# Kernel tuning notes

Measured on AMD Instinct MI355X. Metric: run time of the kernel, lower is better.

Reference implementation:

```python
import jax, jax.numpy as jnp
import numpy as np

N = 10000        # nodes
F_IN = 128       # node features (data.num_node_features)
OUT = 16         # out_channels
H = 32           # attention heads
C1 = 4 * OUT     # hidden per-head dim (4*out_channels)
E = 80000        # directed edges
EPS = 1e-5       # BatchNorm eps
NEG = 0.2        # GATConv LeakyReLU negative_slope


def _gat(x, src, dst, W, a_s, a_d, b, n, C):
    # PyG GATConv, shared lin, concat=False (mean over heads)
    h = (x @ W).reshape(n, H, C)                    # [n,H,C]
    e_src = jnp.sum(h * a_s, -1)                    # [n,H] (alpha from x_j)
    e_dst = jnp.sum(h * a_d, -1)                    # [n,H] (alpha from x_i)
    e = jax.nn.leaky_relu(e_src[src] + e_dst[dst], NEG)     # [E',H]
    m = jax.ops.segment_max(e, dst, num_segments=n)         # segment softmax
    p = jnp.exp(e - m[dst])
    z = jax.ops.segment_sum(p, dst, num_segments=n)
    alpha = p / z[dst]
    out = jax.ops.segment_sum(alpha[:, :, None] * h[src], dst, num_segments=n)
    return out.mean(1) + b                          # mean over heads + bias


def _bn(x, g, b, m, v):  # eval-mode BatchNorm1d (running stats)
    return (x - m) * g / jnp.sqrt(v + EPS) + b


def setup_inputs():
    k = jax.random.split(jax.random.key(0), 40)
    rn = lambda i, s, sc=0.1: jax.random.normal(k[i], s, jnp.float32) * sc
    d = {"x": jax.random.normal(k[0], (N, F_IN), jnp.float32),
         "edge_index": jax.random.randint(k[1], (2, E), 0, N, jnp.int32)}
    # 4 GATConv layers
    d.update(W1=rn(2, (F_IN, H * C1)), as1=rn(3, (H, C1)), ad1=rn(4, (H, C1)), b1=rn(5, (C1,)))
    d.update(W2=rn(6, (C1, H * OUT)), as2=rn(7, (H, OUT)), ad2=rn(8, (H, OUT)), b2=rn(9, (OUT,)))
    d.update(W3=rn(10, (F_IN, H * C1)), as3=rn(11, (H, C1)), ad3=rn(12, (H, C1)), b3=rn(13, (C1,)))
    d.update(W4=rn(14, (C1, H * OUT)), as4=rn(15, (H, OUT)), ad4=rn(16, (H, OUT)), b4=rn(17, (OUT,)))
    # ResidualNetwork(1 block): 1x1 Conv1d over L=1 == matmul
    d.update(rwa=rn(18, (F_IN, OUT)), rba=rn(19, (OUT,)),
             bn1g=jnp.ones(OUT), bn1b=jnp.zeros(OUT), bn1m=rn(20, (OUT,)), bn1v=jnp.abs(rn(21, (OUT,))) + 1.0,
             rwb=rn(22, (OUT, OUT)), rbb=rn(23, (OUT,)),
             bn2g=jnp.ones(OUT), bn2b=jnp.zeros(OUT), bn2m=rn(24, (OUT,)), bn2v=jnp.abs(rn(25, (OUT,))) + 1.0,
             wsc=rn(26, (F_IN, OUT)), bsc=rn(27, (OUT,)),
             bnsg=jnp.ones(OUT), bnsb=jnp.zeros(OUT), bnsm=rn(28, (OUT,)), bnsv=jnp.abs(rn(29, (OUT,))) + 1.0,
             wfc=rn(30, (OUT, OUT)), bfc=rn(31, (OUT,)))
    return d


def reference(x, edge_index, W1, as1, ad1, b1, W2, as2, ad2, b2,
              W3, as3, ad3, b3, W4, as4, ad4, b4,
              rwa, rba, bn1g, bn1b, bn1m, bn1v, rwb, rbb, bn2g, bn2b, bn2m, bn2v,
              wsc, bsc, bnsg, bnsb, bnsm, bnsv, wfc, bfc):
    n = x.shape[0]
    loops = jnp.arange(n, dtype=edge_index.dtype)  # add_self_loops=True
    s2t_src = jnp.concatenate([edge_index[0], loops])  # flow source_to_target
    s2t_dst = jnp.concatenate([edge_index[1], loops])
    t2s_src = jnp.concatenate([edge_index[1], loops])  # flow target_to_source
    t2s_dst = jnp.concatenate([edge_index[0], loops])
    # dropout in original is unassigned (no-op); eval mode assumed
    x_s = jax.nn.elu(_gat(x, s2t_src, s2t_dst, W1, as1, ad1, b1, n, C1))
    x_in = jax.nn.elu(_gat(x_s, s2t_src, s2t_dst, W2, as2, ad2, b2, n, OUT))
    x_t = jax.nn.elu(_gat(x, t2s_src, t2s_dst, W3, as3, ad3, b3, n, C1))
    x_out = jax.nn.elu(_gat(x_t, t2s_src, t2s_dst, W4, as4, ad4, b4, n, OUT))
    # ResidualNetwork: block + identity avg-pool (L=1) + fc
    h = jax.nn.relu(_bn(x @ rwa + rba, bn1g, bn1b, bn1m, bn1v))
    h = _bn(h @ rwb + rbb, bn2g, bn2b, bn2m, bn2v)
    sc = _bn(x @ wsc + bsc, bnsg, bnsb, bnsm, bnsv)
    x_self = jax.nn.relu(h + sc) @ wfc + bfc
    return (x_in, x_out, x_self)
```

## Files before the change

### kernel.cpp

```cpp
#include <hip/hip_runtime.h>
#include <stdint.h>

__device__ __forceinline__ float bf2f(unsigned short u) {
  union { unsigned int i; float f; } v; v.i = ((unsigned int)u) << 16; return v.f;
}
__device__ __forceinline__ unsigned short f2bf(float f) {
  union { float f; unsigned int i; } v; v.f = f;
  unsigned int i = v.i;
  unsigned int r = (i + 0x7fffu + ((i >> 16) & 1u)) >> 16;
  return (unsigned short)r;
}

typedef __bf16 bf16x8 __attribute__((ext_vector_type(8)));
typedef float f32x4 __attribute__((ext_vector_type(4)));
typedef float f32x2 __attribute__((ext_vector_type(2)));
union ABfrag { int4 i4; bf16x8 v; };

#if __has_builtin(__builtin_amdgcn_cvt_pk_fp8_f32) && __has_builtin(__builtin_amdgcn_cvt_pk_f32_fp8)
#define HW_FP8 1
#else
#define HW_FP8 0
#endif

__device__ __forceinline__ unsigned char f2fp8_sw(float f) {
  union { float f; unsigned int u; } v; v.f = f;
  unsigned int s = (v.u >> 24) & 0x80;
  float a = fabsf(f);
  if (a >= 448.f) return (unsigned char)(s | 0x7E);
  v.f = a;
  int ex = (int)(v.u >> 23);
  unsigned int man = v.u & 0x7FFFFFu;
  if (ex >= 121) {
    unsigned int val = ((unsigned int)(ex - 120) << 3) | (man >> 20);
    unsigned int rem = man & 0xFFFFFu;
    if (rem > 0x80000u || (rem == 0x80000u && (val & 1))) val++;
    if (val > 0x7E) val = 0x7E;
    return (unsigned char)(s | val);
  }
  int q = (int)(a * 512.f + 0.5f);
  if (q > 8) q = 8;
  return (unsigned char)(s | (unsigned int)q);
}
__device__ __forceinline__ float fp8dec_sw(unsigned char c) {
  unsigned int e = (c >> 3) & 15u, m = c & 7u;
  float v;
  if (e) { union { unsigned int u; float f; } x; x.u = ((e + 120) << 23) | (m << 20); v = x.f; }
  else v = (float)m * 0.001953125f;
  return (c & 0x80) ? -v : v;
}
__device__ __forceinline__ unsigned char f2fp8(float f) {
#if HW_FP8
  int v = __builtin_amdgcn_cvt_pk_fp8_f32(f, f, 0, false);
  return (unsigned char)(v & 0xFF);
#else
  return f2fp8_sw(f);
#endif
}
__device__ __forceinline__ void dec16p(int4 g, f32x2 o[8]) {
#if HW_FP8
  o[0] = __builtin_amdgcn_cvt_pk_f32_fp8(g.x, false);
  o[1] = __builtin_amdgcn_cvt_pk_f32_fp8(g.x, true);
  o[2] = __builtin_amdgcn_cvt_pk_f32_fp8(g.y, false);
  o[3] = __builtin_amdgcn_cvt_pk_f32_fp8(g.y, true);
  o[4] = __builtin_amdgcn_cvt_pk_f32_fp8(g.z, false);
  o[5] = __builtin_amdgcn_cvt_pk_f32_fp8(g.z, true);
  o[6] = __builtin_amdgcn_cvt_pk_f32_fp8(g.w, false);
  o[7] = __builtin_amdgcn_cvt_pk_f32_fp8(g.w, true);
#else
  unsigned int w[4] = {(unsigned)g.x, (unsigned)g.y, (unsigned)g.z, (unsigned)g.w};
#pragma unroll
  for (int d = 0; d < 4; ++d) {
    unsigned int x = w[d];
    o[d * 2 + 0] = (f32x2){fp8dec_sw((unsigned char)(x & 0xFF)),
                           fp8dec_sw((unsigned char)((x >> 8) & 0xFF))};
    o[d * 2 + 1] = (f32x2){fp8dec_sw((unsigned char)((x >> 16) & 0xFF)),
                           fp8dec_sw((unsigned char)((x >> 24) & 0xFF))};
  }
#endif
}

__device__ __forceinline__ float lrelu_clamp(float e) {
  e = (e > 0.f) ? e : 0.2f * e;
  return fminf(e, 80.f);
}

__global__ __launch_bounds__(256) void k_detect(const unsigned int* __restrict__ x, int* flag,
                                                int* __restrict__ degAB, int ndeg2) {
  if (blockIdx.x == 0) {
    __shared__ int cnt;
    if (threadIdx.x == 0) cnt = 0;
    __syncthreads();
    int c = 0;
    for (int i = threadIdx.x; i < 1024; i += 256) {
      unsigned int lo = x[i] & 0xFFFFu;
      int ex = (int)((lo >> 7) & 0xFF);
      if (ex >= 100 && ex <= 140) c++;
    }
    atomicAdd(&cnt, c);
    __syncthreads();
    if (threadIdx.x == 0) flag[0] = (cnt > 600) ? 1 : 0;
    return;
  }
  for (int idx = (blockIdx.x - 1) * 256 + threadIdx.x; idx < ndeg2; idx += 8 * 256) degAB[idx] = 0;
}

struct PrepDesc {
  const void* csrc[32]; float* cdst[32]; int cn[32];
  const void* x; float* xc; unsigned short* xp;
  const void* W1; const void* W2; const void* W3; const void* W4;
  unsigned short* P1; unsigned short* P2; unsigned short* P3; unsigned short* P4;
  int* degAB;
  const int* ei;
  int nxb, xtotal, ctotal, E, nn;
};
__global__ __launch_bounds__(256) void k_prep(PrepDesc d, const int* __restrict__ flag) {
  int isbf = *flag;
  int b = blockIdx.x;
  if (b < d.nxb) {
    int i = b * 256 + threadIdx.x;
    if (i < d.xtotal) {
      float v = isbf ? bf2f(((const unsigned short*)d.x)[i]) : ((const float*)d.x)[i];
      d.xc[i] = v;
      int row = i >> 7, c = i & 127;
      int tm = row >> 4, mr = row & 15;
      int s = c >> 5, quad = (c >> 3) & 3, j = c & 7;
      size_t idx = (((size_t)tm * 4 + s) * 64 + quad * 16 + mr) * 8 + j;
      d.xp[idx] = f2bf(v);
    }
    return;
  }
  b -= d.nxb;
  if (b < 288) {
    int u = b * 256 + threadIdx.x;
    const void* W; unsigned short* P; int K, N, lu;
    if (u < 32768)      { W = d.W1; P = d.P1; K = 128; N = 2048; lu = u; }
    else if (u < 36864) { W = d.W2; P = d.P2; K = 64;  N = 512;  lu = u - 32768; }
    else if (u < 69632) { W = d.W3; P = d.P3; K = 128; N = 2048; lu = u - 36864; }
    else                { W = d.W4; P = d.P4; K = 64;  N = 512;  lu = u - 69632; }
    int ksteps = K >> 5;
    int g = lu / (ksteps * 64);
    int rem = lu - g * (ksteps * 64);
    int s = rem >> 6, lane = rem & 63;
    int mr = lane & 15, quad = lane >> 4;
    int col = g * 16 + mr;
    int kbase = s * 32 + quad * 8;
#pragma unroll
    for (int j = 0; j < 8; ++j) {
      size_t src = (size_t)(kbase + j) * N + col;
      float v = isbf ? bf2f(((const unsigned short*)W)[src]) : ((const float*)W)[src];
      P[(size_t)lu * 8 + j] = f2bf(v);
    }
    return;
  }
  b -= 288;
  if (b < 4) {
    for (int idx = b * 256 + threadIdx.x; idx < d.ctotal; idx += 4 * 256) {
      int t = 0, off = idx;
      while (off >= d.cn[t]) { off -= d.cn[t]; ++t; }
      float v = isbf ? bf2f(((const unsigned short*)d.csrc[t])[off])
                     : ((const float*)d.csrc[t])[off];
      d.cdst[t][off] = v;
    }
    return;
  }
  b -= 4;
  {
    int e = b * 256 + threadIdx.x;
    if (e < d.E) {
      atomicAdd(&d.degAB[d.ei[d.E + e]], 1);
      atomicAdd(&d.degAB[d.nn + d.ei[e]], 1);
    }
  }
}

__global__ __launch_bounds__(1024) void k_exscan2(const int* __restrict__ degA, const int* __restrict__ degB,
                                                  int* __restrict__ rowA, int* __restrict__ rowB,
                                                  int* __restrict__ colA, int* __restrict__ colB,
                                                  int* __restrict__ curA, int* __restrict__ curB, int n) {
  const int* deg = (blockIdx.x == 0) ? degA : degB;
  int* row = (blockIdx.x == 0) ? rowA : rowB;
  int* colx = (blockIdx.x == 0) ? colA : colB;
  int* curx = (blockIdx.x == 0) ? curA : curB;
  __shared__ int wsum[16], wbase[16];
  __shared__ int carry;
  if (threadIdx.x == 0) carry = 0;
  __syncthreads();
  int lane = threadIdx.x & 63, w = threadIdx.x >> 6;
  int chunks = (n + 1023) >> 10;
  for (int ch = 0; ch < chunks; ++ch) {
    int i = (ch << 10) + threadIdx.x;
    int v = (i < n) ? deg[i] : 0;
    int sc = v;
#pragma unroll
    for (int o = 1; o < 64; o <<= 1) { int t = __shfl_up(sc, o); if (lane >= o) sc += t; }
    if (lane == 63) wsum[w] = sc;
    __syncthreads();
    if (threadIdx.x < 16) {
      int v2 = wsum[threadIdx.x], s2 = v2;
#pragma unroll
      for (int o = 1; o < 16; o <<= 1) { int t = __shfl_up(s2, o); if (lane >= o) s2 += t; }
      wbase[threadIdx.x] = s2 - v2;
      if (threadIdx.x == 15) wsum[15] = s2;
    }
    __syncthreads();
    if (i < n) {
      int rv = carry + wbase[w] + (sc - v) + i;
      row[i] = rv;
      colx[rv] = i;
      curx[i] = rv + 1;
    }
    __syncthreads();
    if (threadIdx.x == 0) carry += wsum[15];
    __syncthreads();
  }
  if (threadIdx.x == 0) row[n] = carry + n;
}

union SMem {
  struct { int4 a[1024]; unsigned char tile[4][16][64]; } mm;
  struct { float xs[16][128]; float ha[16][16]; float tt[16][16]; } res;
};

template<int CH, int KSTEPS>
__device__ __forceinline__ void mm_es64_body(int rg, int cg, int MT,
    const unsigned short* __restrict__ Ap, const unsigned short* __restrict__ Bp,
    unsigned char* __restrict__ C, const float* __restrict__ a_s, const float* __restrict__ a_d,
    float* __restrict__ es, float* __restrict__ ed, int N, SMem* sm) {
  const int TI = KSTEPS * 64;
  int vt = MT - rg * 4; if (vt > 4) vt = 4;
  {
    const int4* src = (const int4*)(Ap + (size_t)rg * 4 * TI * 8);
    int tot = vt * TI;
    for (int t = threadIdx.x; t < tot; t += 256) sm->mm.a[t] = src[t];
  }
  __syncthreads();
  int wid = threadIdx.x >> 6;
  int tn = cg * 4 + wid;
  int lane = threadIdx.x & 63;
  int mr = lane & 15, quad = lane >> 4;
  const unsigned short* bp = Bp + ((size_t)tn * 4 * KSTEPS) * 512 + lane * 8;
  f32x4 acc[4][4];
#pragma unroll
  for (int rt = 0; rt < 4; ++rt)
#pragma unroll
    for (int nt = 0; nt < 4; ++nt) acc[rt][nt] = (f32x4){0.f, 0.f, 0.f, 0.f};
#pragma unroll
  for (int s = 0; s < KSTEPS; ++s) {
    ABfrag bfr[4];
#pragma unroll
    for (int nt = 0; nt < 4; ++nt) bfr[nt].i4 = *(const int4*)(bp + (size_t)(nt * KSTEPS + s) * 512);
    ABfrag afr[4];
#pragma unroll
    for (int rt = 0; rt < 4; ++rt) afr[rt].i4 = sm->mm.a[rt * TI + s * 64 + lane];
#pragma unroll
    for (int nt = 0; nt < 4; ++nt)
#pragma unroll
      for (int rt = 0; rt < 4; ++rt)
        acc[rt][nt] = __builtin_amdgcn_mfma_f32_16x16x32_bf16(afr[rt].v, bfr[nt].v, acc[rt][nt], 0, 0, 0);
  }
  int r16 = lane >> 2, seg = lane & 3;
#pragma unroll
  for (int rt = 0; rt < 4; ++rt) {
    if (rt < vt) {
      int tm = rg * 4 + rt;
#pragma unroll
      for (int nt = 0; nt < 4; ++nt)
#pragma unroll
        for (int r = 0; r < 4; ++r)
          sm->mm.tile[wid][quad * 4 + r][nt * 16 + mr] = f2fp8(acc[rt][nt][r]);
      int4 val = *(const int4*)&sm->mm.tile[wid][r16][seg * 16];
      *(int4*)(C + (size_t)(tm * 16 + r16) * N + tn * 64 + seg * 16) = val;
    }
  }
  if (CH == 64) {
    const float* asr = a_s + tn * 64;
    const float* adr = a_d + tn * 64;
    float ws[4], wd[4];
#pragma unroll
    for (int nt = 0; nt < 4; ++nt) { ws[nt] = asr[nt * 16 + mr]; wd[nt] = adr[nt * 16 + mr]; }
#pragma unroll
    for (int rt = 0; rt < 4; ++rt) {
      if (rt < vt) {
        int tm = rg * 4 + rt;
        float pes[4] = {0.f,0.f,0.f,0.f}, ped[4] = {0.f,0.f,0.f,0.f};
#pragma unroll
        for (int nt = 0; nt < 4; ++nt)
#pragma unroll
          for (int r = 0; r < 4; ++r) { pes[r] += acc[rt][nt][r] * ws[nt]; ped[r] += acc[rt][nt][r] * wd[nt]; }
#pragma unroll
        for (int m = 1; m < 16; m <<= 1)
#pragma unroll
          for (int r = 0; r < 4; ++r) {
            pes[r] += __shfl_xor(pes[r], m);
            ped[r] += __shfl_xor(ped[r], m);
          }
        if (mr == 0) {
#pragma unroll
          for (int r = 0; r < 4; ++r) {
            int row = tm * 16 + quad * 4 + r;
            es[row * 32 + tn] = pes[r];
            ed[row * 32 + tn] = ped[r];
          }
        }
      }
    }
  } else {
    float ws[4], wd[4];
#pragma unroll
    for (int nt = 0; nt < 4; ++nt) {
      ws[nt] = a_s[(tn * 4 + nt) * 16 + mr];
      wd[nt] = a_d[(tn * 4 + nt) * 16 + mr];
    }
#pragma unroll
    for (int rt = 0; rt < 4; ++rt) {
      if (rt < vt) {
        int tm = rg * 4 + rt;
        float pes[4][4], ped[4][4];
#pragma unroll
        for (int nt = 0; nt < 4; ++nt)
#pragma unroll
          for (int r = 0; r < 4; ++r) { pes[nt][r] = acc[rt][nt][r] * ws[nt]; ped[nt][r] = acc[rt][nt][r] * wd[nt]; }
#pragma unroll
        for (int m = 1; m < 16; m <<= 1)
#pragma unroll
          for (int nt = 0; nt < 4; ++nt)
#pragma unroll
            for (int r = 0; r < 4; ++r) {
              pes[nt][r] += __shfl_xor(pes[nt][r], m);
              ped[nt][r] += __shfl_xor(ped[nt][r], m);
            }
        if (mr == 0) {
#pragma unroll
          for (int nt = 0; nt < 4; ++nt)
#pragma unroll
            for (int r = 0; r < 4; ++r) {
              int row = tm * 16 + quad * 4 + r;
              es[row * 32 + tn * 4 + nt] = pes[nt][r];
              ed[row * 32 + tn * 4 + nt] = ped[nt][r];
            }
        }
      }
    }
  }
}

struct MM13Desc {
  const unsigned short* Ap;
  const unsigned short* B1; const unsigned short* B3;
  unsigned char* C1; unsigned char* C3;
  const float* as1; const float* ad1; const float* as3; const float* ad3;
  float* es1; float* ed1; float* es3; float* ed3;
  int sblks, mmblks, E, mt;
  const int* ei; int* colA; int* colB; int* curA; int* curB;
  const float* xc;
  const float* rp[20];
  void* outbase; size_t eoff; int n;
  const int* flag;
};
__global__ __launch_bounds__(256) void k_mm13res(MM13Desc d) {
  __shared__ SMem sm;
  int b = blockIdx.x;
  if (b < d.sblks) {
    int e = b * 256 + threadIdx.x;
    if (e < d.E) {
      int s = d.ei[e], dd = d.ei[d.E + e];
      d.colA[atomicAdd(&d.curA[dd], 1)] = s;
      d.colB[atomicAdd(&d.curB[s], 1)] = dd;
    }
    return;
  }
  b -= d.sblks;
  if (b < d.mmblks) {
    mm_es64_body<64,4>(b >> 3, b & 7, d.mt, d.Ap, d.B1, d.C1, d.as1, d.ad1, d.es1, d.ed1, 2048, &sm);
    return;
  }
  b -= d.mmblks;
  if (b < d.mmblks) {
    mm_es64_body<64,4>(b >> 3, b & 7, d.mt, d.Ap, d.B3, d.C3, d.as3, d.ad3, d.es3, d.ed3, 2048, &sm);
    return;
  }
  b -= d.mmblks;
  int nodebase = b * 16;
  for (int t = threadIdx.x; t < 16 * 128; t += 256)
    sm.res.xs[t >> 7][t & 127] = d.xc[(size_t)(nodebase + (t >> 7)) * 128 + (t & 127)];
  __syncthreads();
  int ni = threadIdx.x >> 4, c = threadIdx.x & 15;
  const float* rwa = d.rp[0]; const float* rba = d.rp[1];
  const float* bn1g = d.rp[2]; const float* bn1b = d.rp[3];
  const float* bn1m = d.rp[4]; const float* bn1v = d.rp[5];
  const float* rwb = d.rp[6]; const float* rbb = d.rp[7];
  const float* bn2g = d.rp[8]; const float* bn2b = d.rp[9];
  const float* bn2m = d.rp[10]; const float* bn2v = d.rp[11];
  const float* wsc = d.rp[12]; const float* bsc = d.rp[13];
  const float* bnsg = d.rp[14]; const float* bnsb = d.rp[15];
  const float* bnsm = d.rp[16]; const float* bnsv = d.rp[17];
  const float* wfc = d.rp[18]; const float* bfc = d.rp[19];
  float ya = 0.f, ysc = 0.f;
  for (int k = 0; k < 128; ++k) {
    float xv = sm.res.xs[ni][k];
    ya  += xv * rwa[k * 16 + c];
    ysc += xv * wsc[k * 16 + c];
  }
  ya += rba[c]; ysc += bsc[c];
  float s1 = bn1g[c] * rsqrtf(bn1v[c] + 1e-5f);
  ya = (ya - bn1m[c]) * s1 + bn1b[c];
  ya = fmaxf(ya, 0.f);
  float ss = bnsg[c] * rsqrtf(bnsv[c] + 1e-5f);
  ysc = (ysc - bnsm[c]) * ss + bnsb[c];
  sm.res.ha[ni][c] = ya;
  __syncthreads();
  float h2 = rbb[c];
  for (int k = 0; k < 16; ++k) h2 += sm.res.ha[ni][k] * rwb[k * 16 + c];
  float s2 = bn2g[c] * rsqrtf(bn2v[c] + 1e-5f);
  h2 = (h2 - bn2m[c]) * s2 + bn2b[c];
  sm.res.tt[ni][c] = fmaxf(h2 + ysc, 0.f);
  __syncthreads();
  float o = bfc[c];
  for (int k = 0; k < 16; ++k) o += sm.res.tt[ni][k] * wfc[k * 16 + c];
  size_t oo = d.eoff + (size_t)(nodebase + ni) * 16 + c;
  if (*d.flag) ((unsigned short*)d.outbase)[oo] = f2bf(o);
  else         ((float*)d.outbase)[oo] = o;
}

__global__ __launch_bounds__(256) void k_g64(const unsigned char* __restrict__ h1,
                                             const unsigned char* __restrict__ h3,
                                             const float* __restrict__ es1, const float* __restrict__ ed1,
                                             const float* __restrict__ es3, const float* __restrict__ ed3,
                                             const int* __restrict__ rowA, const int* __restrict__ colA,
                                             const int* __restrict__ rowB, const int* __restrict__ colB,
                                             const float* __restrict__ b1, const float* __restrict__ b3,
                                             unsigned short* __restrict__ xsp, unsigned short* __restrict__ xtp,
                                             int n, int gb) {
  int b = blockIdx.x;
  const unsigned char* h; const float *es, *ed, *bias; const int *rowp, *col; unsigned short* outp;
  if (b < gb) { h = h1; es = es1; ed = ed1; rowp = rowA; col = colA; bias = b1; outp = xsp; }
  else { b -= gb; h = h3; es = es3; ed = ed3; rowp = rowB; col = colB; bias = b3; outp = xtp; }
  int wid = threadIdx.x >> 6, lane = threadIdx.x & 63;
  int i = b * 4 + wid;
  if (i >= n) return;
  int hd0 = lane >> 2, hd1 = 16 + hd0;
  float e0 = ed[i * 32 + hd0];
  float e1 = ed[i * 32 + hd1];
  int beg = rowp[i], end = rowp[i + 1];
  int deg = end - beg;
  int colv = (lane < deg) ? col[beg + lane] : 0;
  f32x2 acc0[8], acc1[8];
#pragma unroll
  for (int k = 0; k < 8; ++k) { acc0[k] = (f32x2){0.f, 0.f}; acc1[k] = (f32x2){0.f, 0.f}; }
  float Z0 = 0.f, Z1 = 0.f;
  int s0 = __shfl(colv, 0);
  const int4* hp0 = (const int4*)(h + (size_t)s0 * 2048);
  int4 ng0 = hp0[lane];
  int4 ng1 = hp0[64 + lane];
  float na = es[s0 * 32 + hd0];
  float nb = es[s0 * 32 + hd1];
  for (int j = 0; j < deg; ++j) {
    int4 g0 = ng0, g1 = ng1;
    float ea = na, eb = nb;
    int jn = j + 1;
    if (jn < deg) {
      int sn = (jn < 64) ? __shfl(colv, jn) : col[beg + jn];
      const int4* hq = (const int4*)(h + (size_t)sn * 2048);
      ng0 = hq[lane];
      ng1 = hq[64 + lane];
      na = es[sn * 32 + hd0];
      nb = es[sn * 32 + hd1];
    }
    float q0 = __expf(lrelu_clamp(ea + e0));
    float q1 = __expf(lrelu_clamp(eb + e1));
    Z0 += q0; Z1 += q1;
    f32x2 d0[8], d1[8];
    dec16p(g0, d0); dec16p(g1, d1);
    f32x2 q0v = (f32x2){q0, q0}, q1v = (f32x2){q1, q1};
#pragma unroll
    for (int k = 0; k < 8; ++k) {
      acc0[k] = __builtin_elementwise_fma(q0v, d0[k], acc0[k]);
      acc1[k] = __builtin_elementwise_fma(q1v, d1[k], acc1[k]);
    }
  }
  float zi0 = 1.0f / Z0, zi1 = 1.0f / Z1;
  f32x2 zi0v = (f32x2){zi0, zi0}, zi1v = (f32x2){zi1, zi1};
  f32x2 v2[8];
#pragma unroll
  for (int k = 0; k < 8; ++k)
    v2[k] = __builtin_elementwise_fma(acc1[k], zi1v, acc0[k] * zi0v);
#pragma unroll
  for (int m = 4; m < 64; m <<= 1)
#pragma unroll
    for (int k = 0; k < 8; ++k) {
      v2[k].x += __shfl_xor(v2[k].x, m);
      v2[k].y += __shfl_xor(v2[k].y, m);
    }
  if (lane < 4) {
    float v[16];
#pragma unroll
    for (int k = 0; k < 8; ++k) { v[2 * k] = v2[k].x; v[2 * k + 1] = v2[k].y; }
    int tm = i >> 4, mr = i & 15;
    unsigned short ob[16];
#pragma unroll
    for (int k = 0; k < 16; ++k) {
      float t = v[k] * (1.f / 32.f) + bias[lane * 16 + k];
      t = (t > 0.f) ? t : (__expf(t) - 1.f);
      ob[k] = f2bf(t);
    }
    int s0w = lane >> 1;
#pragma unroll
    for (int g2 = 0; g2 < 2; ++g2) {
      size_t idx = (((size_t)tm * 2 + s0w) * 64 + ((lane & 1) * 2 + g2) * 16 + mr) * 8;
      *(int4*)(outp + idx) = *(const int4*)(ob + g2 * 8);
    }
  }
}

__global__ __launch_bounds__(256) void k_mm24(const unsigned short* __restrict__ xsp,
                                              const unsigned short* __restrict__ xtp,
                                              const unsigned short* __restrict__ W2p,
                                              const unsigned short* __restrict__ W4p,
                                              unsigned char* __restrict__ h2, unsigned char* __restrict__ h4,
                                              const float* __restrict__ as2, const float* __restrict__ ad2,
                                              const float* __restrict__ as4, const float* __restrict__ ad4,
                                              float* __restrict__ es2, float* __restrict__ ed2,
                                              float* __restrict__ es4, float* __restrict__ ed4,
                                              int mmblks, int mt) {
  __shared__ SMem sm;
  int b = blockIdx.x;
  if (b < mmblks)
    mm_es64_body<16,2>(b >> 1, b & 1, mt, xsp, W2p, h2, as2, ad2, es2, ed2, 512, &sm);
  else {
    b -= mmblks;
    mm_es64_body<16,2>(b >> 1, b & 1, mt, xtp, W4p, h4, as4, ad4, es4, ed4, 512, &sm);
  }
}

__global__ __launch_bounds__(256) void k_g16(const unsigned char* __restrict__ h2,
                                             const unsigned char* __restrict__ h4,
                                             const float* __restrict__ es2, const float* __restrict__ ed2,
                                             const float* __restrict__ es4, const float* __restrict__ ed4,
                                             const int* __restrict__ rowA, const int* __restrict__ colA,
                                             const int* __restrict__ rowB, const int* __restrict__ colB,
                                             const float* __restrict__ b2, const float* __restrict__ b4,
                                             void* __restrict__ outbase, int n, int gb,
                                             const int* __restrict__ flag) {
  int b = blockIdx.x;
  const unsigned char* h; const float *es, *ed, *bias; const int *rowp, *col; size_t eoff;
  if (b < gb) { h = h2; es = es2; ed = ed2; rowp = rowA; col = colA; bias = b2; eoff = 0; }
  else { b -= gb; h = h4; es = es4; ed = ed4; rowp = rowB; col = colB; bias = b4; eoff = (size_t)n * 16; }
  int wid = threadIdx.x >> 6, lane = threadIdx.x & 63;
  int i = b * 4 + wid;
  if (i >= n) return;
  int hh = lane & 31, j2 = lane >> 5;
  float ev = ed[i * 32 + hh];
  int beg = rowp[i], end = rowp[i + 1];
  int deg = end - beg;
  int colv = (lane < deg) ? col[beg + lane] : 0;
  f32x2 acc[8];
#pragma unroll
  for (int k = 0; k < 8; ++k) acc[k] = (f32x2){0.f, 0.f};
  float Z = 0.f;
  int j = j2;
  int4 ng = (int4){0, 0, 0, 0};
  float ne = 0.f;
  if (j < deg) {
    int s = __shfl(colv, j);
    ng = ((const int4*)(h + (size_t)s * 512))[hh];
    ne = es[s * 32 + hh];
  }
  for (; j < deg; j += 2) {
    int4 g = ng; float ee = ne;
    int jn = j + 2;
    if (jn < deg) {
      int sn = (jn < 64) ? __shfl(colv, jn) : col[beg + jn];
      ng = ((const int4*)(h + (size_t)sn * 512))[hh];
      ne = es[sn * 32 + hh];
    }
    float q = __expf(lrelu_clamp(ee + ev));
    Z += q;
    f32x2 d[8];
    dec16p(g, d);
    f32x2 qv = (f32x2){q, q};
#pragma unroll
    for (int k = 0; k < 8; ++k) acc[k] = __builtin_elementwise_fma(qv, d[k], acc[k]);
  }
  Z += __shfl_xor(Z, 32);
  float zi = 1.0f / Z;
  f32x2 ziv = (f32x2){zi, zi};
  f32x2 v2[8];
#pragma unroll
  for (int k = 0; k < 8; ++k) v2[k] = acc[k] * ziv;
#pragma unroll
  for (int m = 1; m < 64; m <<= 1)
#pragma unroll
    for (int k = 0; k < 8; ++k) {
      v2[k].x += __shfl_xor(v2[k].x, m);
      v2[k].y += __shfl_xor(v2[k].y, m);
    }
  if (lane == 0) {
    float v[16];
#pragma unroll
    for (int k = 0; k < 8; ++k) { v[2 * k] = v2[k].x; v[2 * k + 1] = v2[k].y; }
    int isbf = *flag;
    if (isbf) {
      unsigned short ob[16];
#pragma unroll
      for (int k = 0; k < 16; ++k) {
        float t = v[k] * (1.f / 32.f) + bias[k];
        t = (t > 0.f) ? t : (__expf(t) - 1.f);
        ob[k] = f2bf(t);
      }
      unsigned short* o = (unsigned short*)outbase + eoff + (size_t)i * 16;
      *(int4*)o = *(const int4*)ob;
      *(int4*)(o + 8) = *(const int4*)(ob + 8);
    } else {
      float* o = (float*)outbase + eoff + (size_t)i * 16;
#pragma unroll
      for (int k = 0; k < 16; ++k) {
        float t = v[k] * (1.f / 32.f) + bias[k];
        t = (t > 0.f) ? t : (__expf(t) - 1.f);
        o[k] = t;
      }
    }
  }
}

extern "C" void kernel_launch(void* const* d_in, const int* in_sizes, int n_in,
                              void* d_out, int out_size, void* d_ws, size_t ws_size,
                              hipStream_t stream) {
  const int n = in_sizes[0] / 128;
  const int E = in_sizes[1] / 2;
  const int* ei = (const int*)d_in[1];

  char* wsp = (char*)d_ws; size_t off = 0;
  auto alloc = [&](size_t bytes) -> void* {
    void* p = wsp + off; off = (off + bytes + 255) & ~(size_t)255; return p;
  };
  int* flag = (int*)alloc(4);
  float* xc = (float*)alloc((size_t)n * 128 * 4);
  unsigned short* xp = (unsigned short*)alloc((size_t)n * 128 * 2);
  unsigned short* W1p = (unsigned short*)alloc((size_t)2048 * 128 * 2);
  unsigned short* W2p = (unsigned short*)alloc((size_t)512 * 64 * 2);
  unsigned short* W3p = (unsigned short*)alloc((size_t)2048 * 128 * 2);
  unsigned short* W4p = (unsigned short*)alloc((size_t)512 * 64 * 2);
  unsigned char* h1 = (unsigned char*)alloc((size_t)n * 2048);
  unsigned char* h3 = (unsigned char*)alloc((size_t)n * 2048);
  unsigned char* h2 = (unsigned char*)alloc((size_t)n * 512);
  unsigned char* h4 = (unsigned char*)alloc((size_t)n * 512);
  float* es1 = (float*)alloc((size_t)n * 32 * 4);
  float* ed1 = (float*)alloc((size_t)n * 32 * 4);
  float* es3 = (float*)alloc((size_t)n * 32 * 4);
  float* ed3 = (float*)alloc((size_t)n * 32 * 4);
  float* es2 = (float*)alloc((size_t)n * 32 * 4);
  float* ed2 = (float*)alloc((size_t)n * 32 * 4);
  float* es4 = (float*)alloc((size_t)n * 32 * 4);
  float* ed4 = (float*)alloc((size_t)n * 32 * 4);
  unsigned short* xsp = (unsigned short*)alloc((size_t)n * 64 * 2);
  unsigned short* xtp = (unsigned short*)alloc((size_t)n * 64 * 2);
  int* rowA = (int*)alloc((size_t)(n + 1) * 4);
  int* rowB = (int*)alloc((size_t)(n + 1) * 4);
  int* colA = (int*)alloc((size_t)(E + n) * 4);
  int* colB = (int*)alloc((size_t)(E + n) * 4);
  int* degAB = (int*)alloc((size_t)2 * n * 4);
  int* degA = degAB, * degB = degAB + n;
  int* curA = (int*)alloc((size_t)n * 4);
  int* curB = (int*)alloc((size_t)n * 4);

  static const int cidx[32] = {3,4,5, 7,8,9, 11,12,13, 15,16,17,
                               18,19,20,21,22,23,24,25,26,27,28,29,
                               30,31,32,33,34,35,36,37};
  PrepDesc pd;
  float* canon[38] = {nullptr};
  pd.ctotal = 0;
  for (int t = 0; t < 32; ++t) {
    int ii = cidx[t];
    canon[ii] = (float*)alloc((size_t)in_sizes[ii] * 4);
    pd.csrc[t] = d_in[ii];
    pd.cdst[t] = canon[ii];
    pd.cn[t] = in_sizes[ii];
    pd.ctotal += in_sizes[ii];
  }
  pd.x = d_in[0]; pd.xc = xc; pd.xp = xp;
  pd.W1 = d_in[2]; pd.W2 = d_in[6]; pd.W3 = d_in[10]; pd.W4 = d_in[14];
  pd.P1 = W1p; pd.P2 = W2p; pd.P3 = W3p; pd.P4 = W4p;
  pd.degAB = degAB;
  pd.ei = ei;
  pd.nxb = (n * 128 + 255) / 256;
  pd.xtotal = n * 128;
  pd.E = E;
  pd.nn = n;
  (void)ws_size; (void)n_in; (void)out_size;

  const int degblks = (E + 255) / 256;

  k_detect<<<9, 256, 0, stream>>>((const unsigned int*)d_in[0], flag, degAB, 2 * n);
  k_prep<<<pd.nxb + 288 + 4 + degblks, 256, 0, stream>>>(pd, flag);
  k_exscan2<<<2, 1024, 0, stream>>>(degA, degB, rowA, rowB, colA, colB, curA, curB, n);

  const int mt = n / 16;
  const int nrg = (mt + 3) / 4;
  const int mmblks64 = nrg * 8;
  const int mmblks16 = nrg * 2;
  const int gb = (n + 3) / 4;

  MM13Desc md;
  md.Ap = xp; md.B1 = W1p; md.B3 = W3p; md.C1 = h1; md.C3 = h3;
  md.as1 = canon[3]; md.ad1 = canon[4]; md.as3 = canon[11]; md.ad3 = canon[12];
  md.es1 = es1; md.ed1 = ed1; md.es3 = es3; md.ed3 = ed3;
  md.sblks = degblks; md.mmblks = mmblks64; md.E = E; md.mt = mt;
  md.ei = ei; md.colA = colA; md.colB = colB; md.curA = curA; md.curB = curB;
  md.xc = xc;
  for (int t = 0; t < 20; ++t) md.rp[t] = canon[18 + t];
  md.outbase = d_out; md.eoff = (size_t)2 * n * 16; md.n = n; md.flag = flag;
  k_mm13res<<<degblks + 2 * mmblks64 + mt, 256, 0, stream>>>(md);

  k_g64<<<2 * gb, 256, 0, stream>>>(h1, h3, es1, ed1, es3, ed3,
                                    rowA, colA, rowB, colB,
                                    canon[5], canon[13], xsp, xtp, n, gb);
  k_mm24<<<2 * mmblks16, 256, 0, stream>>>(xsp, xtp, W2p, W4p, h2, h4,
                                           canon[7], canon[8], canon[15], canon[16],
                                           es2, ed2, es4, ed4, mmblks16, mt);
  k_g16<<<2 * gb, 256, 0, stream>>>(h2, h4, es2, ed2, es4, ed4,
                                    rowA, colA, rowB, colB,
                                    canon[9], canon[17], d_out, n, gb, flag);
}
```

Measured before the change: 327.6 us.

## Vectorize x prep, load MFMA A-fragments directly, reorder fused kernel blocks

The x conversion/packing in k_prep now has each thread handle 8 contiguous elements, using vector loads and stores instead of scalar ones. The GEMM body no longer stages the A tile into shared memory with a barrier; each lane loads its A fragments straight from global memory, which shrinks the shared-memory union and may raise occupancy. The residual-network blocks move to the front of the fused launch so that small, latency-bound work is scheduled first rather than trailing the GEMMs. The trade-off is redundant global loads of A across the warps in a block, which now rely on cache rather than on one shared copy.

```diff
diff --git a/kernel.cpp b/kernel.cpp
--- a/kernel.cpp
+++ b/kernel.cpp
@@ -117,15 +117,31 @@
   int isbf = *flag;
   int b = blockIdx.x;
   if (b < d.nxb) {
-    int i = b * 256 + threadIdx.x;
-    if (i < d.xtotal) {
-      float v = isbf ? bf2f(((const unsigned short*)d.x)[i]) : ((const float*)d.x)[i];
-      d.xc[i] = v;
-      int row = i >> 7, c = i & 127;
+    int t8 = b * 256 + threadIdx.x;
+    int i8 = t8 * 8;
+    if (i8 < d.xtotal) {
+      float v[8];
+      if (isbf) {
+        int4 raw = *(const int4*)((const unsigned short*)d.x + i8);
+        const unsigned short* u = (const unsigned short*)&raw;
+#pragma unroll
+        for (int j = 0; j < 8; ++j) v[j] = bf2f(u[j]);
+      } else {
+        float4 f0 = *(const float4*)((const float*)d.x + i8);
+        float4 f1 = *(const float4*)((const float*)d.x + i8 + 4);
+        v[0] = f0.x; v[1] = f0.y; v[2] = f0.z; v[3] = f0.w;
+        v[4] = f1.x; v[5] = f1.y; v[6] = f1.z; v[7] = f1.w;
+      }
+      *(float4*)(d.xc + i8)     = (float4){v[0], v[1], v[2], v[3]};
+      *(float4*)(d.xc + i8 + 4) = (float4){v[4], v[5], v[6], v[7]};
+      int row = i8 >> 7, c0 = i8 & 127;
       int tm = row >> 4, mr = row & 15;
-      int s = c >> 5, quad = (c >> 3) & 3, j = c & 7;
-      size_t idx = (((size_t)tm * 4 + s) * 64 + quad * 16 + mr) * 8 + j;
-      d.xp[idx] = f2bf(v);
+      int s = c0 >> 5, quad = (c0 >> 3) & 3;
+      unsigned short o[8];
+#pragma unroll
+      for (int j = 0; j < 8; ++j) o[j] = f2bf(v[j]);
+      size_t idx = (((size_t)tm * 4 + s) * 64 + quad * 16 + mr) * 8;
+      *(int4*)(d.xp + idx) = *(const int4*)o;
     }
     return;
   }
@@ -217,7 +233,7 @@
 }
 
 union SMem {
-  struct { int4 a[1024]; unsigned char tile[4][16][64]; } mm;
+  unsigned char tile[4][16][64];
   struct { float xs[16][128]; float ha[16][16]; float tt[16][16]; } res;
 };
 
@@ -228,16 +244,11 @@
     float* __restrict__ es, float* __restrict__ ed, int N, SMem* sm) {
   const int TI = KSTEPS * 64;
   int vt = MT - rg * 4; if (vt > 4) vt = 4;
-  {
-    const int4* src = (const int4*)(Ap + (size_t)rg * 4 * TI * 8);
-    int tot = vt * TI;
-    for (int t = threadIdx.x; t < tot; t += 256) sm->mm.a[t] = src[t];
-  }
-  __syncthreads();
   int wid = threadIdx.x >> 6;
   int tn = cg * 4 + wid;
   int lane = threadIdx.x & 63;
   int mr = lane & 15, quad = lane >> 4;
+  const int4* ap = (const int4*)(Ap + (size_t)rg * 4 * TI * 8) + lane;
   const unsigned short* bp = Bp + ((size_t)tn * 4 * KSTEPS) * 512 + lane * 8;
   f32x4 acc[4][4];
 #pragma unroll
@@ -251,7 +262,10 @@
     for (int nt = 0; nt < 4; ++nt) bfr[nt].i4 = *(const int4*)(bp + (size_t)(nt * KSTEPS + s) * 512);
     ABfrag afr[4];
 #pragma unroll
-    for (int rt = 0; rt < 4; ++rt) afr[rt].i4 = sm->mm.a[rt * TI + s * 64 + lane];
+    for (int rt = 0; rt < 4; ++rt) {
+      int rti = (rt < vt) ? rt : 0;
+      afr[rt].i4 = ap[rti * TI + s * 64];
+    }
 #pragma unroll
     for (int nt = 0; nt < 4; ++nt)
 #pragma unroll
@@ -267,8 +281,8 @@
       for (int nt = 0; nt < 4; ++nt)
 #pragma unroll
         for (int r = 0; r < 4; ++r)
-          sm->mm.tile[wid][quad * 4 + r][nt * 16 + mr] = f2fp8(acc[rt][nt][r]);
-      int4 val = *(const int4*)&sm->mm.tile[wid][r16][seg * 16];
+          sm->tile[wid][quad * 4 + r][nt * 16 + mr] = f2fp8(acc[rt][nt][r]);
+      int4 val = *(const int4*)&sm->tile[wid][r16][seg * 16];
       *(int4*)(C + (size_t)(tm * 16 + r16) * N + tn * 64 + seg * 16) = val;
     }
   }
@@ -350,7 +364,7 @@
   unsigned char* C1; unsigned char* C3;
   const float* as1; const float* ad1; const float* as3; const float* ad3;
   float* es1; float* ed1; float* es3; float* ed3;
-  int sblks, mmblks, E, mt;
+  int resblks, sblks, mmblks, E, mt;
   const int* ei; int* colA; int* colB; int* curA; int* curB;
   const float* xc;
   const float* rp[20];
@@ -360,6 +374,53 @@
 __global__ __launch_bounds__(256) void k_mm13res(MM13Desc d) {
   __shared__ SMem sm;
   int b = blockIdx.x;
+  if (b < d.resblks) {
+    int nodebase = b * 16;
+    for (int t = threadIdx.x; t < 16 * 128; t += 256)
+      sm.res.xs[t >> 7][t & 127] = d.xc[(size_t)(nodebase + (t >> 7)) * 128 + (t & 127)];
+    __syncthreads();
+    int ni = threadIdx.x >> 4, c = threadIdx.x & 15;
+    const float* rwa = d.rp[0]; const float* rba = d.rp[1];
+    const float* bn1g = d.rp[2]; const float* bn1b = d.rp[3];
+    const float* bn1m = d.rp[4]; const float* bn1v = d.rp[5];
+    const float* rwb = d.rp[6]; const float* rbb = d.rp[7];
+    const float* bn2g = d.rp[8]; const float* bn2b = d.rp[9];
+    const float* bn2m = d.rp[10]; const float* bn2v = d.rp[11];
+    const float* wsc = d.rp[12]; const float* bsc = d.rp[13];
+    const float* bnsg = d.rp[14]; const float* bnsb = d.rp[15];
+    const float* bnsm = d.rp[16]; const float* bnsv = d.rp[17];
+    const float* wfc = d.rp[18]; const float* bfc = d.rp[19];
+    float ya = 0.f, ysc = 0.f;
+#pragma unroll 8
+    for (int k = 0; k < 128; ++k) {
+      float xv = sm.res.xs[ni][k];
+      ya  += xv * rwa[k * 16 + c];
+      ysc += xv * wsc[k * 16 + c];
+    }
+    ya += rba[c]; ysc += bsc[c];
+    float s1 = bn1g[c] * rsqrtf(bn1v[c] + 1e-5f);
+    ya = (ya - bn1m[c]) * s1 + bn1b[c];
+    ya = fmaxf(ya, 0.f);
+    float ss = bnsg[c] * rsqrtf(bnsv[c] + 1e-5f);
+    ysc = (ysc - bnsm[c]) * ss + bnsb[c];
+    sm.res.ha[ni][c] = ya;
+    __syncthreads();
+    float h2 = rbb[c];
+#pragma unroll
+    for (int k = 0; k < 16; ++k) h2 += sm.res.ha[ni][k] * rwb[k * 16 + c];
+    float s2 = bn2g[c] * rsqrtf(bn2v[c] + 1e-5f);
+    h2 = (h2 - bn2m[c]) * s2 + bn2b[c];
+    sm.res.tt[ni][c] = fmaxf(h2 + ysc, 0.f);
+    __syncthreads();
+    float o = bfc[c];
+#pragma unroll
+    for (int k = 0; k < 16; ++k) o += sm.res.tt[ni][k] * wfc[k * 16 + c];
+    size_t oo = d.eoff + (size_t)(nodebase + ni) * 16 + c;
+    if (*d.flag) ((unsigned short*)d.outbase)[oo] = f2bf(o);
+    else         ((float*)d.outbase)[oo] = o;
+    return;
+  }
+  b -= d.resblks;
   if (b < d.sblks) {
     int e = b * 256 + threadIdx.x;
     if (e < d.E) {
@@ -375,51 +436,7 @@
     return;
   }
   b -= d.mmblks;
-  if (b < d.mmblks) {
-    mm_es64_body<64,4>(b >> 3, b & 7, d.mt, d.Ap, d.B3, d.C3, d.as3, d.ad3, d.es3, d.ed3, 2048, &sm);
-    return;
-  }
-  b -= d.mmblks;
-  int nodebase = b * 16;
-  for (int t = threadIdx.x; t < 16 * 128; t += 256)
-    sm.res.xs[t >> 7][t & 127] = d.xc[(size_t)(nodebase + (t >> 7)) * 128 + (t & 127)];
-  __syncthreads();
-  int ni = threadIdx.x >> 4, c = threadIdx.x & 15;
-  const float* rwa = d.rp[0]; const float* rba = d.rp[1];
-  const float* bn1g = d.rp[2]; const float* bn1b = d.rp[3];
-  const float* bn1m = d.rp[4]; const float* bn1v = d.rp[5];
-  const float* rwb = d.rp[6]; const float* rbb = d.rp[7];
-  const float* bn2g = d.rp[8]; const float* bn2b = d.rp[9];
-  const float* bn2m = d.rp[10]; const float* bn2v = d.rp[11];
-  const float* wsc = d.rp[12]; const float* bsc = d.rp[13];
-  const float* bnsg = d.rp[14]; const float* bnsb = d.rp[15];
-  const float* bnsm = d.rp[16]; const float* bnsv = d.rp[17];
-  const float* wfc = d.rp[18]; const float* bfc = d.rp[19];
-  float ya = 0.f, ysc = 0.f;
-  for (int k = 0; k < 128; ++k) {
-    float xv = sm.res.xs[ni][k];
-    ya  += xv * rwa[k * 16 + c];
-    ysc += xv * wsc[k * 16 + c];
-  }
-  ya += rba[c]; ysc += bsc[c];
-  float s1 = bn1g[c] * rsqrtf(bn1v[c] + 1e-5f);
-  ya = (ya - bn1m[c]) * s1 + bn1b[c];
-  ya = fmaxf(ya, 0.f);
-  float ss = bnsg[c] * rsqrtf(bnsv[c] + 1e-5f);
-  ysc = (ysc - bnsm[c]) * ss + bnsb[c];
-  sm.res.ha[ni][c] = ya;
-  __syncthreads();
-  float h2 = rbb[c];
-  for (int k = 0; k < 16; ++k) h2 += sm.res.ha[ni][k] * rwb[k * 16 + c];
-  float s2 = bn2g[c] * rsqrtf(bn2v[c] + 1e-5f);
-  h2 = (h2 - bn2m[c]) * s2 + bn2b[c];
-  sm.res.tt[ni][c] = fmaxf(h2 + ysc, 0.f);
-  __syncthreads();
-  float o = bfc[c];
-  for (int k = 0; k < 16; ++k) o += sm.res.tt[ni][k] * wfc[k * 16 + c];
-  size_t oo = d.eoff + (size_t)(nodebase + ni) * 16 + c;
-  if (*d.flag) ((unsigned short*)d.outbase)[oo] = f2bf(o);
-  else         ((float*)d.outbase)[oo] = o;
+  mm_es64_body<64,4>(b >> 3, b & 7, d.mt, d.Ap, d.B3, d.C3, d.as3, d.ad3, d.es3, d.ed3, 2048, &sm);
 }
 
 __global__ __launch_bounds__(256) void k_g64(const unsigned char* __restrict__ h1,
@@ -682,7 +699,7 @@
   pd.P1 = W1p; pd.P2 = W2p; pd.P3 = W3p; pd.P4 = W4p;
   pd.degAB = degAB;
   pd.ei = ei;
-  pd.nxb = (n * 128 + 255) / 256;
+  pd.nxb = (n * 128 / 8 + 255) / 256;
   pd.xtotal = n * 128;
   pd.E = E;
   pd.nn = n;
@@ -704,12 +721,12 @@
   md.Ap = xp; md.B1 = W1p; md.B3 = W3p; md.C1 = h1; md.C3 = h3;
   md.as1 = canon[3]; md.ad1 = canon[4]; md.as3 = canon[11]; md.ad3 = canon[12];
   md.es1 = es1; md.ed1 = ed1; md.es3 = es3; md.ed3 = ed3;
-  md.sblks = degblks; md.mmblks = mmblks64; md.E = E; md.mt = mt;
+  md.resblks = mt; md.sblks = degblks; md.mmblks = mmblks64; md.E = E; md.mt = mt;
   md.ei = ei; md.colA = colA; md.colB = colB; md.curA = curA; md.curB = curB;
   md.xc = xc;
   for (int t = 0; t < 20; ++t) md.rp[t] = canon[18 + t];
   md.outbase = d_out; md.eoff = (size_t)2 * n * 16; md.n = n; md.flag = flag;
-  k_mm13res<<<degblks + 2 * mmblks64 + mt, 256, 0, stream>>>(md);
+  k_mm13res<<<mt + degblks + 2 * mmblks64, 256, 0, stream>>>(md);
 
   k_g64<<<2 * gb, 256, 0, stream>>>(h1, h3, es1, ed1, es3, ed3,
                                     rowA, colA, rowB, colB,
```

Result: no change. 323.9 us (-1.1%).
